# Optimization experiments

Measured on AMD Instinct MI355X. Metric: run time of the kernel, lower is better.

## Reference

```python
import jax, jax.numpy as jnp
import numpy as np

LAT = 512
FIN = 256
FOUT = 256
K = 3
N_STYLE = 4
B, H, W = 16, 64, 64


def setup_inputs() -> dict:
    key = jax.random.key(0)
    ks = jax.random.split(key, 8)
    x = jax.random.normal(ks[0], (B, FIN, H, W), dtype=jnp.float32)
    lat = jax.random.normal(ks[1], (B, LAT), dtype=jnp.float32)
    # main conv weight, kaiming_normal fan_in, leaky_relu a=0 -> gain sqrt(2)
    fan_in = FIN * K * K
    weight = jax.random.normal(ks[2], (FOUT, FIN, K, K), dtype=jnp.float32) * np.float32(np.sqrt(2.0 / fan_in))
    # EqualLinear layers: raw weight ~ N(0,1), runtime-scaled by 1/sqrt(in_dim)
    ws = jax.random.normal(ks[3], (N_STYLE, LAT, LAT), dtype=jnp.float32)
    bs = jnp.zeros((N_STYLE, LAT), dtype=jnp.float32)
    # final plain nn.Linear(lat_size, fin): uniform(-1/sqrt(in), 1/sqrt(in))
    bound = np.float32(1.0 / np.sqrt(LAT))
    wf = jax.random.uniform(ks[4], (FIN, LAT), dtype=jnp.float32, minval=-bound, maxval=bound)
    bf = jax.random.uniform(ks[5], (FIN,), dtype=jnp.float32, minval=-bound, maxval=bound)
    return {"x": x, "lat": lat, "weight": weight, "ws": ws, "bs": bs, "wf": wf, "bf": bf}


def reference(x, lat, weight, ws, bs, wf, bf):
    Bb, fin, Hh, Ww = x.shape
    fout, _, k, _ = weight.shape
    eq_scale = np.float32(1.0 / np.sqrt(lat.shape[1]))  # EqualLinear runtime scale

    # style MLP: n_layers_style x (EqualLinear + LeakyReLU(0.2)), then Linear -> fin
    h = lat
    for i in range(ws.shape[0]):
        h = jax.nn.leaky_relu(h @ (ws[i] * eq_scale).T + bs[i], 0.2)
    styles = h @ wf.T + bf  # [B, fin]

    # normalize base weight by inf-norm over (fin,k,k) per output channel
    wnorm = jnp.max(jnp.abs(weight), axis=(1, 2, 3), keepdims=True)
    mw = weight * (np.float32(1.0 / np.sqrt(fin * k * k)) / wnorm)  # [fout,fin,k,k]
    # normalize styles by inf-norm per sample
    styles = styles / jnp.max(jnp.abs(styles), axis=1, keepdims=True)

    # per-sample modulation + demodulation
    w = mw[None] * styles[:, None, :, None, None]  # [B,fout,fin,k,k]
    dcoefs = jax.lax.rsqrt(jnp.sum(w * w, axis=(2, 3, 4)) + 1e-8)  # [B,fout]
    w = w * dcoefs[:, :, None, None, None]
    w = w.reshape(Bb * fout, fin, k, k)

    # grouped conv with groups = batch (stride/dilation NOT passed in original -> 1)
    pad = (k - 1) // 2  # _get_same_padding with stride=1, dilation=1
    xg = x.reshape(1, Bb * fin, Hh, Ww)
    y = jax.lax.conv_general_dilated(
        xg, w, window_strides=(1, 1), padding=[(pad, pad), (pad, pad)],
        dimension_numbers=("NCHW", "OIHW", "NCHW"), feature_group_count=Bb)
    return y.reshape(Bb, fout, Hh, Ww)
```

## Files before the change

kernel.cpp:

```cpp
#include <hip/hip_runtime.h>
#include <hip/hip_bf16.h>

#define LATN 512
#define FINN 256
#define FOUTN 256
#define NB 16
#define HH 64
#define WW 64

typedef __attribute__((ext_vector_type(8))) short bf16x8;
typedef __attribute__((ext_vector_type(4))) float f32x4;
typedef __attribute__((ext_vector_type(4))) int i32x4;

#define WS_ZERO   0
#define WS_MW2    4096
#define WS_DCO    266240
#define WS_SNORM  282624
#define WS_WFMT   299008
#define WS_XM     1478656
#define WS_HA     (WS_XM)
#define WS_HB     (WS_XM + 32768)
#define WS_STY    (WS_XM + 65536)

__global__ void weight_prep_kernel(const float* __restrict__ weight,
                                   __hip_bfloat16* __restrict__ wfmt,
                                   float* __restrict__ mw2sum,
                                   float* __restrict__ zerobuf) {
    __shared__ float red[256];
    int o = blockIdx.x, t = threadIdx.x;
    if (o == 0 && t < 64) zerobuf[t] = 0.f;
    const float* wrow = weight + ((size_t)o * FINN + t) * 9;
    float wv[9];
    float mx = 0.f;
    #pragma unroll
    for (int k = 0; k < 9; ++k) { wv[k] = wrow[k]; mx = fmaxf(mx, fabsf(wv[k])); }
    red[t] = mx;
    __syncthreads();
    for (int k = 128; k > 0; k >>= 1) {
        if (t < k) red[t] = fmaxf(red[t], red[t + k]);
        __syncthreads();
    }
    float scale = (1.0f / 48.0f) / red[0];
    int obi = o >> 6, ol = o & 63, ch = t >> 5, il = t & 31;
    int slot = (il >> 3) ^ ((ol >> 1) & 3);
    char* basep = (char*)wfmt + (size_t)obi * 294912 + (size_t)ch * 36864
                + (size_t)ol * 64 + slot * 16 + (il & 7) * 2;
    float s2 = 0.f;
    #pragma unroll
    for (int tap = 0; tap < 9; ++tap) {
        float m = wv[tap] * scale;
        s2 += m * m;
        *(__hip_bfloat16*)(basep + tap * 4096) = __float2bfloat16(m);
    }
    mw2sum[(size_t)o * FINN + t] = s2;
}

__global__ __launch_bounds__(256) void style_layer_kernel(
    const float* __restrict__ in, const float* __restrict__ w,
    const float* __restrict__ bias, float* __restrict__ out,
    int in_dim_v4, int out_dim, float scale, int do_lrelu) {
    int t = threadIdx.x;
    int jl = t >> 4, kl = t & 15;
    int j = blockIdx.x * 16 + jl;
    int b = blockIdx.y;
    const float4* inr = (const float4*)(in + (size_t)b * (in_dim_v4 * 4));
    const float4* wr  = (const float4*)(w + (size_t)j * (in_dim_v4 * 4));
    float sum = 0.f;
    #pragma unroll 4
    for (int kb = kl; kb < in_dim_v4; kb += 16) {
        float4 wv = wr[kb], iv = inr[kb];
        sum += wv.x * iv.x + wv.y * iv.y + wv.z * iv.z + wv.w * iv.w;
    }
    #pragma unroll
    for (int off = 8; off >= 1; off >>= 1)
        sum += __shfl_xor(sum, off, 16);
    if (kl == 0) {
        float v = sum * scale + bias[j];
        if (do_lrelu && v < 0.f) v *= 0.2f;
        out[(size_t)b * out_dim + j] = v;
    }
}

__global__ __launch_bounds__(256) void norm_dcoef_kernel(
    const float* __restrict__ sty, const float* __restrict__ mw2,
    float* __restrict__ snorm, float* __restrict__ dco) {
    __shared__ float red[256];
    __shared__ float s2[256];
    int b = blockIdx.x, t = threadIdx.x;
    float v = sty[(size_t)b * FINN + t];
    red[t] = fabsf(v);
    __syncthreads();
    for (int k = 128; k > 0; k >>= 1) {
        if (t < k) red[t] = fmaxf(red[t], red[t + k]);
        __syncthreads();
    }
    float sv = v / red[0];
    snorm[(size_t)b * FINN + t] = sv;
    s2[t] = sv * sv;
    __syncthreads();
    const float4* m2 = (const float4*)(mw2 + (size_t)t * FINN);
    const float4* sq = (const float4*)s2;
    float sum = 0.f;
    #pragma unroll 8
    for (int kb = 0; kb < 64; ++kb) {
        float4 a = m2[kb], xq = sq[kb];
        sum += a.x * xq.x + a.y * xq.y + a.z * xq.z + a.w * xq.w;
    }
    dco[(size_t)b * FOUTN + t] = rsqrtf(sum + 1e-8f);
}

__global__ __launch_bounds__(256) void xcvt_kernel(const float* __restrict__ x,
                                                   const float* __restrict__ sn,
                                                   char* __restrict__ xm) {
    __shared__ float tile[64][65];
    int h = blockIdx.x, b = blockIdx.y;
    int t = threadIdx.x;
    int wl_ = t & 63, ig = t >> 6;
    char* xmb = xm + (size_t)b * 2097152;
    for (int icb = 0; icb < 4; ++icb) {
        if (icb) __syncthreads();
        #pragma unroll
        for (int p = 0; p < 16; ++p) {
            int i_l = p * 4 + ig;
            int i = icb * 64 + i_l;
            tile[i_l][wl_] = x[((size_t)(b * FINN + i)) * 4096 + h * 64 + wl_]
                             * sn[(size_t)b * FINN + i];
        }
        __syncthreads();
        #pragma unroll
        for (int rep = 0; rep < 2; ++rep) {
            int g = rep * 256 + t;
            int w = g >> 3, q8 = g & 7;
            int chunk = icb * 2 + (q8 >> 2), iq = q8 & 3;
            int slot = iq ^ (((h + 1) + ((w + 1) >> 1)) & 3);
            short tmp[8];
            #pragma unroll
            for (int j = 0; j < 8; ++j) {
                __hip_bfloat16 hb = __float2bfloat16(tile[q8 * 8 + j][w]);
                tmp[j] = *(short*)&hb;
            }
            char* dst = xmb + (size_t)chunk * 262144 + (size_t)(h * 64 + w) * 64 + slot * 16;
            *(bf16x8*)dst = *(bf16x8*)tmp;
        }
    }
}

__device__ __forceinline__ void gl_lds16(const void* g, void* l) {
    __builtin_amdgcn_global_load_lds(
        (const __attribute__((address_space(1))) unsigned int*)g,
        (__attribute__((address_space(3))) unsigned int*)l, 16, 0, 0);
}

__global__ __launch_bounds__(512, 1) void mconv_kernel(
    const char* __restrict__ xm, const char* __restrict__ wfmt,
    const float* __restrict__ dco, float* __restrict__ y) {
    __shared__ char xs[76032];
    __shared__ char wl[2][36864];

    int t = threadIdx.x;
    int lane = t & 63;
    int wid = t >> 6;
    int h0 = blockIdx.x * 16;
    int obi = blockIdx.y;
    int b = blockIdx.z;

    if (t < 144) {
        int r = t >> 3, sub = t & 7;
        int col = (sub >> 2) * 65, slot = sub & 3;
        *(i32x4*)(xs + ((r * 66 + col) * 4 + slot) * 16) = (i32x4){0, 0, 0, 0};
    }
    if (h0 == 0) {
        for (int e = t; e < 256; e += 512)
            *(i32x4*)(xs + ((0 * 66 + 1 + (e >> 2)) * 4 + (e & 3)) * 16) = (i32x4){0, 0, 0, 0};
    }
    if (h0 == 48) {
        for (int e = t; e < 256; e += 512)
            *(i32x4*)(xs + ((17 * 66 + 1 + (e >> 2)) * 4 + (e & 3)) * 16) = (i32x4){0, 0, 0, 0};
    }

    const char* xmb = xm + (size_t)b * 2097152 + lane * 16;
    unsigned xoff[9], xdst[9];
    #pragma unroll
    for (int q = 0; q < 9; ++q) {
        int idx = wid * 9 + q;
        int r = idx >> 2, quarter = idx & 3;
        int gh = h0 - 1 + r;
        bool v = (gh >= 0) && (gh < HH);
        xoff[q] = (unsigned)__builtin_amdgcn_readfirstlane(
            v ? (int)((gh * 64 + quarter * 16) * 64) : (int)0xFFFFFFFF);
        xdst[q] = (unsigned)__builtin_amdgcn_readfirstlane(
            (int)((r * 66 + 1) * 64 + quarter * 1024));
    }
    const char* wlane = wfmt + (size_t)obi * 294912 + lane * 16;

    f32x4 acc[4][8] = {};
    int l15 = lane & 15, lg = lane >> 4;
    int wfrag = l15 * 64 + ((lg ^ ((l15 >> 1) & 3)) << 4);

    #pragma unroll
    for (int q = 0; q < 5; ++q) {
        int idx = wid + q * 8;
        if (idx < 36) gl_lds16(wlane + idx * 1024, wl[0] + idx * 1024);
    }
    wlane += 36864;

    for (int ch = 0; ch < 8; ++ch) {
        int cur = ch & 1;
        const char* xch = xmb + (size_t)ch * 262144;
        #pragma unroll
        for (int q = 0; q < 9; ++q)
            if (xoff[q] != 0xFFFFFFFFu) gl_lds16(xch + xoff[q], xs + xdst[q]);
        if (ch < 7) {
            #pragma unroll
            for (int q = 0; q < 5; ++q) {
                int idx = wid + q * 8;
                if (idx < 36) gl_lds16(wlane + idx * 1024, wl[cur ^ 1] + idx * 1024);
            }
            wlane += 36864;
            if (wid < 4) asm volatile("s_waitcnt vmcnt(5)" ::: "memory");
            else         asm volatile("s_waitcnt vmcnt(4)" ::: "memory");
        } else {
            asm volatile("s_waitcnt vmcnt(0)" ::: "memory");
        }
        asm volatile("s_waitcnt lgkmcnt(0)" ::: "memory");
        __builtin_amdgcn_s_barrier();
        __builtin_amdgcn_sched_barrier(0);

        const char* wlb = wl[cur];
        #pragma unroll
        for (int kh = 0; kh < 3; ++kh) {
            #pragma unroll
            for (int kw = 0; kw < 3; ++kw) {
                int tap = kh * 3 + kw;
                int pa = (wid * 2 + kh) * 66 + kw + l15;
                int pb = pa + 66;
                int xa = pa * 64 + ((lg ^ ((pa >> 1) & 3)) << 4);
                int xb = pb * 64 + ((lg ^ ((pb >> 1) & 3)) << 4);
                bf16x8 wf[4], x0[4], x1[4];
                #pragma unroll
                for (int mt = 0; mt < 4; ++mt)
                    wf[mt] = *(const bf16x8*)(wlb + tap * 4096 + mt * 1024 + wfrag);
                #pragma unroll
                for (int nt = 0; nt < 4; ++nt)
                    x0[nt] = *(const bf16x8*)(xs + xa + nt * 1024);
                #pragma unroll
                for (int nt = 0; nt < 4; ++nt)
                    x1[nt] = *(const bf16x8*)(xs + xb + nt * 1024);
                __builtin_amdgcn_sched_barrier(0);
                asm volatile("s_waitcnt lgkmcnt(4)" ::: "memory");
                __builtin_amdgcn_sched_barrier(0);
                __builtin_amdgcn_s_setprio(1);
                #pragma unroll
                for (int mt = 0; mt < 4; ++mt)
                    #pragma unroll
                    for (int nt = 0; nt < 4; ++nt)
                        acc[mt][nt] = __builtin_amdgcn_mfma_f32_16x16x32_bf16(
                            wf[mt], x0[nt], acc[mt][nt], 0, 0, 0);
                __builtin_amdgcn_s_setprio(0);
                __builtin_amdgcn_sched_barrier(0);
                asm volatile("s_waitcnt lgkmcnt(0)" ::: "memory");
                __builtin_amdgcn_sched_barrier(0);
                __builtin_amdgcn_s_setprio(1);
                #pragma unroll
                for (int mt = 0; mt < 4; ++mt)
                    #pragma unroll
                    for (int nt = 0; nt < 4; ++nt)
                        acc[mt][4 + nt] = __builtin_amdgcn_mfma_f32_16x16x32_bf16(
                            wf[mt], x1[nt], acc[mt][4 + nt], 0, 0, 0);
                __builtin_amdgcn_s_setprio(0);
            }
        }

        __builtin_amdgcn_s_barrier();
        __builtin_amdgcn_sched_barrier(0);
    }

    const float* dcb = dco + (size_t)b * FOUTN + obi * 64;
    #pragma unroll
    for (int rr = 0; rr < 2; ++rr) {
        float* yb = y + (((size_t)b * FOUTN + obi * 64) * HH + (h0 + wid * 2 + rr)) * WW;
        #pragma unroll
        for (int mt = 0; mt < 4; ++mt) {
            #pragma unroll
            for (int j = 0; j < 4; ++j) {
                int o_l = mt * 16 + lg * 4 + j;
                float d = dcb[o_l];
                #pragma unroll
                for (int n4 = 0; n4 < 4; ++n4)
                    yb[(size_t)o_l * 4096 + n4 * 16 + l15] = acc[mt][rr * 4 + n4][j] * d;
            }
        }
    }
}

extern "C" void kernel_launch(void* const* d_in, const int* in_sizes, int n_in,
                              void* d_out, int out_size, void* d_ws, size_t ws_size,
                              hipStream_t stream) {
    const float* x      = (const float*)d_in[0];
    const float* lat    = (const float*)d_in[1];
    const float* weight = (const float*)d_in[2];
    const float* wsm    = (const float*)d_in[3];
    const float* bsm    = (const float*)d_in[4];
    const float* wff    = (const float*)d_in[5];
    const float* bff    = (const float*)d_in[6];
    float* y = (float*)d_out;

    char* base = (char*)d_ws;
    float* zerobuf = (float*)(base + WS_ZERO);
    float* mw2     = (float*)(base + WS_MW2);
    float* dco     = (float*)(base + WS_DCO);
    float* snorm   = (float*)(base + WS_SNORM);
    __hip_bfloat16* wfmt = (__hip_bfloat16*)(base + WS_WFMT);
    char* xm       = base + WS_XM;
    float* hA      = (float*)(base + WS_HA);
    float* hB      = (float*)(base + WS_HB);
    float* sty     = (float*)(base + WS_STY);

    const float eq = 0.044194173824159216f;

    weight_prep_kernel<<<FOUTN, 256, 0, stream>>>(weight, wfmt, mw2, zerobuf);
    style_layer_kernel<<<dim3(LATN / 16, NB), 256, 0, stream>>>(
        lat, wsm + 0 * (size_t)LATN * LATN, bsm + 0 * LATN, hA, LATN / 4, LATN, eq, 1);
    style_layer_kernel<<<dim3(LATN / 16, NB), 256, 0, stream>>>(
        hA, wsm + 1 * (size_t)LATN * LATN, bsm + 1 * LATN, hB, LATN / 4, LATN, eq, 1);
    style_layer_kernel<<<dim3(LATN / 16, NB), 256, 0, stream>>>(
        hB, wsm + 2 * (size_t)LATN * LATN, bsm + 2 * LATN, hA, LATN / 4, LATN, eq, 1);
    style_layer_kernel<<<dim3(LATN / 16, NB), 256, 0, stream>>>(
        hA, wsm + 3 * (size_t)LATN * LATN, bsm + 3 * LATN, hB, LATN / 4, LATN, eq, 1);
    style_layer_kernel<<<dim3(FINN / 16, NB), 256, 0, stream>>>(
        hB, wff, bff, sty, LATN / 4, FINN, 1.0f, 0);
    norm_dcoef_kernel<<<NB, 256, 0, stream>>>(sty, mw2, snorm, dco);
    xcvt_kernel<<<dim3(HH, NB), 256, 0, stream>>>(x, snorm, xm);
    mconv_kernel<<<dim3(4, 4, NB), 512, 0, stream>>>(xm, (const char*)wfmt, dco, y);
}
```

Before: 115.0 us.

## Halve conv block height and drop weight double-buffering for two blocks per CU

Each conv block now covers 8 rows with 256 threads instead of 16 rows with 512. The weight tile is single-buffered, cutting shared memory per block so two blocks fit on a CU, and the grid doubles to 512 blocks. Latency hiding moves from in-block prefetch of the next weight chunk to overlap between co-resident blocks. The trade-off is a full vmcnt(0) wait before every chunk, plus more halo rows reloaded relative to useful rows and each weight chunk fetched by twice as many blocks.

```diff
diff --git a/kernel.cpp b/kernel.cpp
--- a/kernel.cpp
+++ b/kernel.cpp
@@ -151,38 +151,38 @@
         (__attribute__((address_space(3))) unsigned int*)l, 16, 0, 0);
 }
 
-__global__ __launch_bounds__(512, 1) void mconv_kernel(
+__global__ __launch_bounds__(256, 2) void mconv_kernel(
     const char* __restrict__ xm, const char* __restrict__ wfmt,
     const float* __restrict__ dco, float* __restrict__ y) {
-    __shared__ char xs[76032];
-    __shared__ char wl[2][36864];
+    __shared__ char xs[42240];
+    __shared__ char wl[36864];
 
     int t = threadIdx.x;
     int lane = t & 63;
     int wid = t >> 6;
-    int h0 = blockIdx.x * 16;
+    int h0 = blockIdx.x * 8;
     int obi = blockIdx.y;
     int b = blockIdx.z;
 
-    if (t < 144) {
+    if (t < 80) {
         int r = t >> 3, sub = t & 7;
         int col = (sub >> 2) * 65, slot = sub & 3;
         *(i32x4*)(xs + ((r * 66 + col) * 4 + slot) * 16) = (i32x4){0, 0, 0, 0};
     }
     if (h0 == 0) {
-        for (int e = t; e < 256; e += 512)
-            *(i32x4*)(xs + ((0 * 66 + 1 + (e >> 2)) * 4 + (e & 3)) * 16) = (i32x4){0, 0, 0, 0};
-    }
-    if (h0 == 48) {
-        for (int e = t; e < 256; e += 512)
-            *(i32x4*)(xs + ((17 * 66 + 1 + (e >> 2)) * 4 + (e & 3)) * 16) = (i32x4){0, 0, 0, 0};
+        int e = t;
+        *(i32x4*)(xs + ((0 * 66 + 1 + (e >> 2)) * 4 + (e & 3)) * 16) = (i32x4){0, 0, 0, 0};
+    }
+    if (h0 == 56) {
+        int e = t;
+        *(i32x4*)(xs + ((9 * 66 + 1 + (e >> 2)) * 4 + (e & 3)) * 16) = (i32x4){0, 0, 0, 0};
     }
 
     const char* xmb = xm + (size_t)b * 2097152 + lane * 16;
-    unsigned xoff[9], xdst[9];
-    #pragma unroll
-    for (int q = 0; q < 9; ++q) {
-        int idx = wid * 9 + q;
+    unsigned xoff[10], xdst[10];
+    #pragma unroll
+    for (int q = 0; q < 10; ++q) {
+        int idx = wid * 10 + q;
         int r = idx >> 2, quarter = idx & 3;
         int gh = h0 - 1 + r;
         bool v = (gh >= 0) && (gh < HH);
@@ -197,36 +197,19 @@
     int l15 = lane & 15, lg = lane >> 4;
     int wfrag = l15 * 64 + ((lg ^ ((l15 >> 1) & 3)) << 4);
 
-    #pragma unroll
-    for (int q = 0; q < 5; ++q) {
-        int idx = wid + q * 8;
-        if (idx < 36) gl_lds16(wlane + idx * 1024, wl[0] + idx * 1024);
-    }
-    wlane += 36864;
-
     for (int ch = 0; ch < 8; ++ch) {
-        int cur = ch & 1;
         const char* xch = xmb + (size_t)ch * 262144;
         #pragma unroll
+        for (int q = 0; q < 10; ++q)
+            if (xoff[q] != 0xFFFFFFFFu) gl_lds16(xch + xoff[q], xs + xdst[q]);
+        const char* wch = wlane + (size_t)ch * 36864;
+        #pragma unroll
         for (int q = 0; q < 9; ++q)
-            if (xoff[q] != 0xFFFFFFFFu) gl_lds16(xch + xoff[q], xs + xdst[q]);
-        if (ch < 7) {
-            #pragma unroll
-            for (int q = 0; q < 5; ++q) {
-                int idx = wid + q * 8;
-                if (idx < 36) gl_lds16(wlane + idx * 1024, wl[cur ^ 1] + idx * 1024);
-            }
-            wlane += 36864;
-            if (wid < 4) asm volatile("s_waitcnt vmcnt(5)" ::: "memory");
-            else         asm volatile("s_waitcnt vmcnt(4)" ::: "memory");
-        } else {
-            asm volatile("s_waitcnt vmcnt(0)" ::: "memory");
-        }
-        asm volatile("s_waitcnt lgkmcnt(0)" ::: "memory");
+            gl_lds16(wch + (wid + q * 4) * 1024, wl + (wid + q * 4) * 1024);
+        asm volatile("s_waitcnt vmcnt(0) lgkmcnt(0)" ::: "memory");
         __builtin_amdgcn_s_barrier();
         __builtin_amdgcn_sched_barrier(0);
 
-        const char* wlb = wl[cur];
         #pragma unroll
         for (int kh = 0; kh < 3; ++kh) {
             #pragma unroll
@@ -239,7 +222,7 @@
                 bf16x8 wf[4], x0[4], x1[4];
                 #pragma unroll
                 for (int mt = 0; mt < 4; ++mt)
-                    wf[mt] = *(const bf16x8*)(wlb + tap * 4096 + mt * 1024 + wfrag);
+                    wf[mt] = *(const bf16x8*)(wl + tap * 4096 + mt * 1024 + wfrag);
                 #pragma unroll
                 for (int nt = 0; nt < 4; ++nt)
                     x0[nt] = *(const bf16x8*)(xs + xa + nt * 1024);
@@ -331,5 +314,5 @@
         hB, wff, bff, sty, LATN / 4, FINN, 1.0f, 0);
     norm_dcoef_kernel<<<NB, 256, 0, stream>>>(sty, mw2, snorm, dco);
     xcvt_kernel<<<dim3(HH, NB), 256, 0, stream>>>(x, snorm, xm);
-    mconv_kernel<<<dim3(4, 4, NB), 512, 0, stream>>>(xm, (const char*)wfmt, dco, y);
-}
+    mconv_kernel<<<dim3(8, 4, NB), 256, 0, stream>>>(xm, (const char*)wfmt, dco, y);
+}
```

Result: faster. 112.4 us, median of 2 (-2.3%).
